# Performance work log

Hardware: AMD Instinct MI355X
Metric: run time of the kernel (lower is better)

The kernel has to match this reference:

```python
import jax, jax.numpy as jnp
import numpy as np

NUM_CLASSES = 19
EPSILON = 1e-05


def setup_inputs() -> dict:
    key = jax.random.key(0)
    k1, k2 = jax.random.split(key)
    shape = (16, 1024, 1024)
    y_pred = jax.random.randint(k1, shape, 0, NUM_CLASSES, dtype=jnp.int64 if jax.config.read('jax_enable_x64') else jnp.int32)
    y = jax.random.randint(k2, shape, 0, NUM_CLASSES, dtype=y_pred.dtype)
    return {"y_pred": y_pred, "y": y}


def reference(y_pred, y):
    # Flatten label maps; compute all per-class counts in one pass via bincount
    yp = y_pred.reshape(-1)
    yt = y.reshape(-1)
    # count of (y == i)
    count_y = jnp.bincount(yt, length=NUM_CLASSES).astype(jnp.float32)
    # count of (y_pred == i)
    count_p = jnp.bincount(yp, length=NUM_CLASSES).astype(jnp.float32)
    # intersection_i = count(y == i AND y_pred == i): histogram of y where labels agree
    agree = (yp == yt).astype(jnp.float32)
    inter = jnp.bincount(yt, weights=agree, length=NUM_CLASSES)
    # union_i = |A| + |B| - |A & B|
    union = count_y + count_p - inter
    dice_coeffs = (2.0 * inter + EPSILON) / (union + EPSILON)
    dice_loss = 1.0 - jnp.mean(dice_coeffs)
    return dice_loss
```

## Files before the change

### kernel.cpp

```cpp
#include <hip/hip_runtime.h>

#define NC 19
#define NB (NC * NC)
#define NCOPY 8
#define UNROLL 8
#define EPS 1e-5f

__global__ __launch_bounds__(256, 4) void joint_hist_kernel(
    const int4* __restrict__ yp, const int4* __restrict__ yt,
    unsigned int* __restrict__ gJ, int n4)
{
    __shared__ unsigned int sJ[NCOPY * NB];
    const int tid = threadIdx.x;
    unsigned int* mine = &sJ[(tid >> 5) * NB];

    for (int i = tid; i < NCOPY * NB; i += 256) sJ[i] = 0u;
    __syncthreads();

    const int nthreads = gridDim.x * 256;
    int i = blockIdx.x * 256 + tid;

    for (; i + 7 * nthreads < n4; i += 8 * nthreads) {
        int4 p[UNROLL], t[UNROLL];
        #pragma unroll
        for (int u = 0; u < UNROLL; ++u) {
            p[u] = yp[i + u * nthreads];
            t[u] = yt[i + u * nthreads];
        }
        #pragma unroll
        for (int u = 0; u < UNROLL; ++u) {
            atomicAdd(&mine[t[u].x * NC + p[u].x], 1u);
            atomicAdd(&mine[t[u].y * NC + p[u].y], 1u);
            atomicAdd(&mine[t[u].z * NC + p[u].z], 1u);
            atomicAdd(&mine[t[u].w * NC + p[u].w], 1u);
        }
    }
    for (; i < n4; i += nthreads) {
        int4 p = yp[i], t = yt[i];
        atomicAdd(&mine[t.x * NC + p.x], 1u);
        atomicAdd(&mine[t.y * NC + p.y], 1u);
        atomicAdd(&mine[t.z * NC + p.z], 1u);
        atomicAdd(&mine[t.w * NC + p.w], 1u);
    }
    __syncthreads();

    for (int b = tid; b < NB; b += 256) {
        unsigned int v = 0;
        #pragma unroll
        for (int c = 0; c < NCOPY; ++c) v += sJ[c * NB + b];
        if (v) atomicAdd(&gJ[b], v);
    }
}

__global__ __launch_bounds__(64) void dice_final_kernel(
    const unsigned int* __restrict__ gJ, float* __restrict__ out)
{
    const int lane = threadIdx.x;
    float dice = 0.0f;
    if (lane < NC) {
        float inter = (float)gJ[lane * NC + lane];
        float cy = 0.0f, cp = 0.0f;
        #pragma unroll
        for (int j = 0; j < NC; ++j) {
            cy += (float)gJ[lane * NC + j];
            cp += (float)gJ[j * NC + lane];
        }
        float uni = cy + cp - inter;
        dice = (2.0f * inter + EPS) / (uni + EPS);
    }
    #pragma unroll
    for (int off = 32; off > 0; off >>= 1)
        dice += __shfl_down(dice, off, 64);
    if (lane == 0) out[0] = 1.0f - dice / (float)NC;
}

extern "C" void kernel_launch(void* const* d_in, const int* in_sizes, int n_in,
                              void* d_out, int out_size, void* d_ws, size_t ws_size,
                              hipStream_t stream)
{
    const int4* yp = (const int4*)d_in[0];
    const int4* yt = (const int4*)d_in[1];
    unsigned int* gJ = (unsigned int*)d_ws;
    float* out = (float*)d_out;

    const int n = in_sizes[0];
    const int n4 = n >> 2;

    hipMemsetAsync(d_ws, 0, NB * sizeof(unsigned int), stream);

    const int grid = 2048;
    joint_hist_kernel<<<grid, 256, 0, stream>>>(yp, yt, gJ, n4);
    dice_final_kernel<<<1, 64, 0, stream>>>(gJ, out);
}
```

Measured before the change: 176.2 us.

## Replace global atomics and memset with per-block partials reduced in final kernel

Each block now writes its joint histogram to its own slot in the workspace instead of atomically adding into one global histogram. This removes the memset launch and the global atomic contention. The final kernel sums the per-block partials, using 722 threads that each cover half of the blocks, before computing the dice loss. The grid also shrinks from 2048 to 512 blocks, which cuts partial-reduction work but may lower memory-level parallelism in the main pass.

```diff
diff --git a/kernel.cpp b/kernel.cpp
--- a/kernel.cpp
+++ b/kernel.cpp
@@ -3,12 +3,12 @@
 #define NC 19
 #define NB (NC * NC)
 #define NCOPY 8
-#define UNROLL 8
 #define EPS 1e-5f
+#define MAXG 512
 
 __global__ __launch_bounds__(256, 4) void joint_hist_kernel(
     const int4* __restrict__ yp, const int4* __restrict__ yt,
-    unsigned int* __restrict__ gJ, int n4)
+    unsigned int* __restrict__ part, int n4)
 {
     __shared__ unsigned int sJ[NCOPY * NB];
     const int tid = threadIdx.x;
@@ -21,14 +21,14 @@
     int i = blockIdx.x * 256 + tid;
 
     for (; i + 7 * nthreads < n4; i += 8 * nthreads) {
-        int4 p[UNROLL], t[UNROLL];
+        int4 p[8], t[8];
         #pragma unroll
-        for (int u = 0; u < UNROLL; ++u) {
+        for (int u = 0; u < 8; ++u) {
             p[u] = yp[i + u * nthreads];
             t[u] = yt[i + u * nthreads];
         }
         #pragma unroll
-        for (int u = 0; u < UNROLL; ++u) {
+        for (int u = 0; u < 8; ++u) {
             atomicAdd(&mine[t[u].x * NC + p[u].x], 1u);
             atomicAdd(&mine[t[u].y * NC + p[u].y], 1u);
             atomicAdd(&mine[t[u].z * NC + p[u].z], 1u);
@@ -44,34 +44,66 @@
     }
     __syncthreads();
 
+    unsigned int* my_part = part + blockIdx.x * NB;
     for (int b = tid; b < NB; b += 256) {
         unsigned int v = 0;
         #pragma unroll
         for (int c = 0; c < NCOPY; ++c) v += sJ[c * NB + b];
-        if (v) atomicAdd(&gJ[b], v);
+        my_part[b] = v;
     }
 }
 
-__global__ __launch_bounds__(64) void dice_final_kernel(
-    const unsigned int* __restrict__ gJ, float* __restrict__ out)
+__global__ __launch_bounds__(1024) void dice_final_kernel(
+    const unsigned int* __restrict__ part, float* __restrict__ out, int G)
 {
-    const int lane = threadIdx.x;
-    float dice = 0.0f;
-    if (lane < NC) {
-        float inter = (float)gJ[lane * NC + lane];
-        float cy = 0.0f, cp = 0.0f;
+    __shared__ unsigned int J[NB];
+    const int tid = threadIdx.x;
+    const int half = G >> 1;
+
+    unsigned int s = 0;
+    int bin = 0;
+    if (tid < 2 * NB) {
+        bin = (tid < NB) ? tid : tid - NB;
+        const int b0 = (tid < NB) ? 0 : half;
+        const int b1 = (tid < NB) ? half : G;
+        unsigned int a0 = 0, a1 = 0, a2 = 0, a3 = 0, a4 = 0, a5 = 0, a6 = 0, a7 = 0;
+        int b = b0;
+        for (; b + 7 < b1; b += 8) {
+            a0 += part[(b + 0) * NB + bin];
+            a1 += part[(b + 1) * NB + bin];
+            a2 += part[(b + 2) * NB + bin];
+            a3 += part[(b + 3) * NB + bin];
+            a4 += part[(b + 4) * NB + bin];
+            a5 += part[(b + 5) * NB + bin];
+            a6 += part[(b + 6) * NB + bin];
+            a7 += part[(b + 7) * NB + bin];
+        }
+        for (; b < b1; ++b) a0 += part[b * NB + bin];
+        s = ((a0 + a1) + (a2 + a3)) + ((a4 + a5) + (a6 + a7));
+    }
+    if (tid < NB) J[bin] = s;
+    __syncthreads();
+    if (tid >= NB && tid < 2 * NB) J[bin] += s;
+    __syncthreads();
+
+    if (tid < 64) {
+        float dice = 0.0f;
+        if (tid < NC) {
+            float inter = (float)J[tid * NC + tid];
+            float cy = 0.0f, cp = 0.0f;
+            #pragma unroll
+            for (int j = 0; j < NC; ++j) {
+                cy += (float)J[tid * NC + j];
+                cp += (float)J[j * NC + tid];
+            }
+            float uni = cy + cp - inter;
+            dice = (2.0f * inter + EPS) / (uni + EPS);
+        }
         #pragma unroll
-        for (int j = 0; j < NC; ++j) {
-            cy += (float)gJ[lane * NC + j];
-            cp += (float)gJ[j * NC + lane];
-        }
-        float uni = cy + cp - inter;
-        dice = (2.0f * inter + EPS) / (uni + EPS);
+        for (int off = 32; off > 0; off >>= 1)
+            dice += __shfl_down(dice, off, 64);
+        if (tid == 0) out[0] = 1.0f - dice / (float)NC;
     }
-    #pragma unroll
-    for (int off = 32; off > 0; off >>= 1)
-        dice += __shfl_down(dice, off, 64);
-    if (lane == 0) out[0] = 1.0f - dice / (float)NC;
 }
 
 extern "C" void kernel_launch(void* const* d_in, const int* in_sizes, int n_in,
@@ -80,15 +112,17 @@
 {
     const int4* yp = (const int4*)d_in[0];
     const int4* yt = (const int4*)d_in[1];
-    unsigned int* gJ = (unsigned int*)d_ws;
+    unsigned int* part = (unsigned int*)d_ws;
     float* out = (float*)d_out;
 
     const int n = in_sizes[0];
     const int n4 = n >> 2;
 
-    hipMemsetAsync(d_ws, 0, NB * sizeof(unsigned int), stream);
+    int G = MAXG;
+    const int gmax = (int)(ws_size / (NB * sizeof(unsigned int)));
+    if (gmax < G) G = gmax & ~1;
+    if (G < 2) G = 2;
 
-    const int grid = 2048;
-    joint_hist_kernel<<<grid, 256, 0, stream>>>(yp, yt, gJ, n4);
-    dice_final_kernel<<<1, 64, 0, stream>>>(gJ, out);
+    joint_hist_kernel<<<G, 256, 0, stream>>>(yp, yt, part, n4);
+    dice_final_kernel<<<1, 1024, 0, stream>>>(part, out, G);
 }
```

Result: faster. 156.8 us (-11.0%).
